# Kernel optimization log

Measured on AMD Instinct MI355X. Metric: run time of the kernel, lower is better.

## Reference

```python
import jax, jax.numpy as jnp
import numpy as np

DIM = 768
HEADS = 12
HEAD_DIM = DIM // HEADS
HIDDEN = 4 * DIM


def layer_norm(x, g, b, eps=1e-5):
    mu = jnp.mean(x, axis=-1, keepdims=True)
    var = jnp.var(x, axis=-1, keepdims=True)
    return (x - mu) * jax.lax.rsqrt(var + eps) * g + b


def setup_inputs() -> dict:
    key = jax.random.key(0)
    ks = jax.random.split(key, 8)
    s = lambda fan_in: 1.0 / np.sqrt(fan_in)
    return {
        "x": jax.random.normal(ks[0], (16, 577, DIM), dtype=jnp.float32),
        "ln1_g": jnp.ones((DIM,), jnp.float32),
        "ln1_b": jnp.zeros((DIM,), jnp.float32),
        "w_qkv": jax.random.uniform(ks[1], (DIM, 3 * DIM), jnp.float32, -s(DIM), s(DIM)),
        "b_qkv": jnp.zeros((3 * DIM,), jnp.float32),
        "w_proj": jax.random.uniform(ks[2], (DIM, DIM), jnp.float32, -s(DIM), s(DIM)),
        "b_proj": jnp.zeros((DIM,), jnp.float32),
        "ln2_g": jnp.ones((DIM,), jnp.float32),
        "ln2_b": jnp.zeros((DIM,), jnp.float32),
        "w_fc1": jax.random.uniform(ks[3], (DIM, HIDDEN), jnp.float32, -s(DIM), s(DIM)),
        "b_fc1": jnp.zeros((HIDDEN,), jnp.float32),
        "w_fc2": jax.random.uniform(ks[4], (HIDDEN, DIM), jnp.float32, -s(HIDDEN), s(HIDDEN)),
        "b_fc2": jnp.zeros((DIM,), jnp.float32),
    }


def reference(x, ln1_g, ln1_b, w_qkv, b_qkv, w_proj, b_proj,
              ln2_g, ln2_b, w_fc1, b_fc1, w_fc2, b_fc2):
    B, N, C = x.shape
    scale = HEAD_DIM ** -0.5

    # --- attention branch (pre-norm) ---
    h = layer_norm(x, ln1_g, ln1_b)
    qkv = h @ w_qkv + b_qkv                               # [B,N,3C]
    qkv = qkv.reshape(B, N, 3, HEADS, HEAD_DIM)
    q, k, v = [qkv[:, :, i].transpose(0, 2, 1, 3) for i in range(3)]  # [B,H,N,D]
    attn = jnp.einsum("bhnd,bhmd->bhnm", q, k) * scale
    attn = jax.nn.softmax(attn, axis=-1)
    out = jnp.einsum("bhnm,bhmd->bhnd", attn, v)          # [B,H,N,D]
    out = out.transpose(0, 2, 1, 3).reshape(B, N, C)
    x = x + (out @ w_proj + b_proj)

    # --- MLP branch (pre-norm) ---
    h = layer_norm(x, ln2_g, ln2_b)
    h = jax.nn.gelu(h @ w_fc1 + b_fc1, approximate=False)
    x = x + (h @ w_fc2 + b_fc2)
    return x
```

## Files before the change

kernel.cpp:

```cpp
#include <hip/hip_runtime.h>
#include <hip/hip_bf16.h>
#include <math.h>

#define NB   16
#define NTOK 577
#define CDIM 768
#define NH   12
#define HID  3072
#define RTOT (NB*NTOK)
#define RPAD (((RTOT+127)/128)*128)
#define BH   (NB*NH)
#define QT   40
#define KF_C (CDIM/32)

typedef __attribute__((ext_vector_type(8))) short bf16x8;
typedef __attribute__((ext_vector_type(4))) float f32x4;
typedef unsigned short u16;

__device__ inline void load_lds16(const void* g, void* l) {
    __builtin_amdgcn_global_load_lds(
        (const __attribute__((address_space(1))) unsigned*)g,
        (__attribute__((address_space(3))) unsigned*)l, 16, 0, 0);
}

__device__ inline size_t blobA(int m, int c, int Kf) {
    return ((size_t)(m >> 4) * Kf + (c >> 5)) * 512 +
           (((c >> 3) & 3) * 16 + (m & 15)) * 8 + (c & 7);
}

__device__ inline float fast_gelu(float x) {
    float y = 0.7978845608f * (x + 0.044715f * x * x * x);
    float e = __expf(2.0f * y);
    float th = 1.0f - 2.0f / (e + 1.0f);
    return 0.5f * x * (1.0f + th);
}

__global__ __launch_bounds__(256) void wconvert_blob(
    const float* __restrict__ src, u16* __restrict__ dst, int K, int N)
{
    int n  = blockIdx.x * 256 + threadIdx.x;
    int kp = blockIdx.y;
    const float* s = src + (size_t)(kp * 8) * N + n;
    __hip_bfloat16 h0 = __float2bfloat16(s[0 * N]);
    __hip_bfloat16 h1 = __float2bfloat16(s[1 * N]);
    __hip_bfloat16 h2 = __float2bfloat16(s[2 * N]);
    __hip_bfloat16 h3 = __float2bfloat16(s[3 * N]);
    __hip_bfloat16 h4 = __float2bfloat16(s[4 * N]);
    __hip_bfloat16 h5 = __float2bfloat16(s[5 * N]);
    __hip_bfloat16 h6 = __float2bfloat16(s[6 * N]);
    __hip_bfloat16 h7 = __float2bfloat16(s[7 * N]);
    ushort4 a = make_ushort4(*(u16*)&h0, *(u16*)&h1, *(u16*)&h2, *(u16*)&h3);
    ushort4 b = make_ushort4(*(u16*)&h4, *(u16*)&h5, *(u16*)&h6, *(u16*)&h7);
    u16* d = dst + ((size_t)(n >> 4) * (K >> 5) + (kp >> 2)) * 512 +
             ((kp & 3) * 16 + (n & 15)) * 8;
    *(ushort4*)(d)     = a;
    *(ushort4*)(d + 4) = b;
}

__global__ __launch_bounds__(256) void ln_kernel(
    const float* __restrict__ x, const float* __restrict__ g,
    const float* __restrict__ b, u16* __restrict__ out)
{
    int row = blockIdx.x;
    const float* xr = x + (size_t)row * CDIM;
    int t = threadIdx.x;
    float v0 = xr[t], v1 = xr[t + 256], v2 = xr[t + 512];
    float s  = v0 + v1 + v2;
    float s2 = v0*v0 + v1*v1 + v2*v2;
    #pragma unroll
    for (int off = 32; off; off >>= 1) {
        s  += __shfl_xor(s, off);
        s2 += __shfl_xor(s2, off);
    }
    __shared__ float red[10];
    int wave = t >> 6, lane = t & 63;
    if (lane == 0) { red[wave] = s; red[wave + 4] = s2; }
    __syncthreads();
    if (t == 0) {
        float ts  = red[0] + red[1] + red[2] + red[3];
        float ts2 = red[4] + red[5] + red[6] + red[7];
        float mu  = ts * (1.0f / CDIM);
        float var = ts2 * (1.0f / CDIM) - mu * mu;
        red[8] = mu;
        red[9] = rsqrtf(var + 1e-5f);
    }
    __syncthreads();
    float mu = red[8], rs = red[9];
    #pragma unroll
    for (int i = 0; i < 3; ++i) {
        int c = t + i * 256;
        float v = (i == 0 ? v0 : (i == 1 ? v1 : v2));
        __hip_bfloat16 hb = __float2bfloat16((v - mu) * rs * g[c] + b[c]);
        out[blobA(row, c, KF_C)] = *(u16*)&hb;
    }
}

template<int TM>
__global__ __launch_bounds__(64) void flat_gemm(
    const u16* __restrict__ Ab, const u16* __restrict__ Bb,
    const float* __restrict__ bias, const float* __restrict__ res,
    void* __restrict__ outv,
    u16* __restrict__ Qp, u16* __restrict__ Kp, u16* __restrict__ Vp,
    int M, int Nc, int K, int nb, int mb, int flags)
{
    __shared__ u16 sb[TM * 1024];
    int lane = threadIdx.x & 63;
    int fr = lane & 15, fq = lane >> 4;

    int fid = blockIdx.x;
    int xcd = fid & 7, w = fid >> 3;
    int slab, n;
    if (flags & 16) {
        int nslab = (mb + 7) >> 3;
        n = w / nslab; slab = w - n * nslab;
    } else {
        slab = w / nb; n = w - slab * nb;
    }
    int m = slab * 8 + xcd;
    if (m >= mb) return;
    int m0 = m * (TM * 16), n0 = n * 64;

    int Kf = K >> 5;
    size_t tstr = (size_t)Kf * 512;
    const u16* Ap = Ab + (size_t)(m0 >> 4) * tstr + lane * 8;
    const u16* Bp = Bb + (size_t)(n0 >> 4) * tstr + lane * 8;

    f32x4 acc[TM][4];
    #pragma unroll
    for (int i = 0; i < TM; ++i)
        #pragma unroll
        for (int j = 0; j < 4; ++j) acc[i][j] = (f32x4){0.f, 0.f, 0.f, 0.f};

#define PF_LD(Abuf, Bbuf, OFF) do {                                          \
    _Pragma("unroll")                                                        \
    for (int tm = 0; tm < TM; ++tm)                                          \
        Abuf[tm] = *(const bf16x8*)(Ap + tm * tstr + (OFF));                 \
    _Pragma("unroll")                                                        \
    for (int tn = 0; tn < 4; ++tn)                                           \
        Bbuf[tn] = *(const bf16x8*)(Bp + tn * tstr + (OFF));                 \
} while (0)

#define PF_FM(Abuf, Bbuf) do {                                               \
    _Pragma("unroll")                                                        \
    for (int tm = 0; tm < TM; ++tm)                                          \
        _Pragma("unroll")                                                    \
        for (int tn = 0; tn < 4; ++tn)                                       \
            acc[tm][tn] = __builtin_amdgcn_mfma_f32_16x16x32_bf16(           \
                Abuf[tm], Bbuf[tn], acc[tm][tn], 0, 0, 0);                   \
} while (0)

    bf16x8 A0[TM], B0[4], A1[TM], B1[4], A2[TM], B2[4];
    PF_LD(A0, B0, 0);
    PF_LD(A1, B1, 512);
    for (int kf = 0; kf < Kf; kf += 3) {
        size_t base = (size_t)kf * 512;
        PF_LD(A2, B2, base + 1024); PF_FM(A0, B0);
        PF_LD(A0, B0, base + 1536); PF_FM(A1, B1);
        PF_LD(A1, B1, base + 2048); PF_FM(A2, B2);
    }
#undef PF_LD
#undef PF_FM

    float* outf = (float*)outv;
    u16* outblob = (u16*)outv;
    int gelu = flags & 1;
    int KfO = Nc >> 5;

    if (flags & 8) {
        int sec = n0 / CDIM;
        int h   = (n0 % CDIM) / 64;
        #pragma unroll
        for (int tm = 0; tm < TM; ++tm) {
            #pragma unroll
            for (int rg = 0; rg < 4; ++rg) {
                int gm = m0 + tm * 16 + fq * 4 + rg;
                if (gm >= M) continue;
                int b   = gm / NTOK;
                int row = gm - b * NTOK;
                int bh  = b * NH + h;
                #pragma unroll
                for (int tn = 0; tn < 4; ++tn) {
                    int d = tn * 16 + fr;
                    float v = acc[tm][tn][rg] + bias[n0 + tn * 16 + fr];
                    __hip_bfloat16 hb = __float2bfloat16(v);
                    if (sec == 0) {
                        Qp[(size_t)(bh * QT + (row >> 4)) * 1024 + (d >> 5) * 512 +
                           (((d >> 3) & 3) * 16 + (row & 15)) * 8 + (d & 7)] = *(u16*)&hb;
                    } else if (sec == 1) {
                        Kp[(size_t)(bh * QT + (row >> 4)) * 1024 + (d >> 5) * 512 +
                           (((d >> 3) & 3) * 16 + (row & 15)) * 8 + (d & 7)] = *(u16*)&hb;
                    } else {
                        Vp[((size_t)(bh * 4 + (d >> 4)) * 20 + (row >> 5)) * 512 +
                           (((row >> 3) & 3) * 16 + (d & 15)) * 8 + (row & 7)] = *(u16*)&hb;
                    }
                }
            }
        }
        return;
    }

    if (flags & 4) {
        #pragma unroll
        for (int tm = 0; tm < TM; ++tm)
            #pragma unroll
            for (int tn = 0; tn < 4; ++tn)
                #pragma unroll
                for (int rg = 0; rg < 4; ++rg) {
                    int cl = tn * 16 + fr;
                    float v = acc[tm][tn][rg] + bias[n0 + cl];
                    if (gelu) v = fast_gelu(v);
                    __hip_bfloat16 hb = __float2bfloat16(v);
                    sb[tm * 1024 + (cl >> 5) * 512 +
                       (((cl >> 3) & 3) * 16 + fq * 4 + rg) * 8 + (cl & 7)] = *(u16*)&hb;
                }
        #pragma unroll
        for (int tm = 0; tm < TM; ++tm) {
            u16* dst = outblob + ((size_t)((m0 >> 4) + tm) * KfO + (n0 >> 5)) * 512;
            *(bf16x8*)(dst + lane * 16)     = *(const bf16x8*)(sb + tm * 1024 + lane * 16);
            *(bf16x8*)(dst + lane * 16 + 8) = *(const bf16x8*)(sb + tm * 1024 + lane * 16 + 8);
        }
        return;
    }

    #pragma unroll
    for (int tm = 0; tm < TM; ++tm) {
        #pragma unroll
        for (int rg = 0; rg < 4; ++rg) {
            int gm = m0 + tm * 16 + fq * 4 + rg;
            if (gm >= M) continue;
            #pragma unroll
            for (int tn = 0; tn < 4; ++tn) {
                int gn = n0 + tn * 16 + fr;
                float v = acc[tm][tn][rg] + bias[gn];
                if (gelu) v = fast_gelu(v);
                if (res)  v += res[(size_t)gm * Nc + gn];
                outf[(size_t)gm * Nc + gn] = v;
            }
        }
    }
}

__global__ __launch_bounds__(256) void attn_mfma(
    const u16* __restrict__ Qp, const u16* __restrict__ Kp,
    const u16* __restrict__ Vp, u16* __restrict__ outp)
{
    __shared__ __align__(16) u16 Ks[4096];
    __shared__ __align__(16) u16 Vs[4096];
    __shared__ __align__(16) u16 Ps[4 * 16 * 72];

    int bh = blockIdx.y, qc = blockIdx.x;
    int b = bh / NH, h = bh % NH;
    int t = threadIdx.x, lane = t & 63, wv = t >> 6;
    int fr = lane & 15, fq = lane >> 4;

    int mt = qc * 4 + wv;
    const u16* qbase = Qp + (size_t)(bh * QT + mt) * 1024 + lane * 8;
    bf16x8 qf0 = *(const bf16x8*)(qbase);
    bf16x8 qf1 = *(const bf16x8*)(qbase + 512);

    const u16* kg = Kp + (size_t)bh * (QT * 1024) + wv * 1024 + lane * 8;
    const u16* vg = Vp + ((size_t)(bh * 4 + wv) * 20) * 512 + lane * 8;
    u16* lK  = Ks + wv * 1024;
    u16* lV  = Vs + wv * 1024;
    u16* psw = Ps + wv * (16 * 72);

    f32x4 o[4];
    float m_r[4], l_r[4];
    #pragma unroll
    for (int i = 0; i < 4; ++i) {
        o[i] = (f32x4){0.f, 0.f, 0.f, 0.f};
        m_r[i] = -1e30f; l_r[i] = 0.f;
    }

    for (int kt = 0; kt < 10; ++kt) {
        load_lds16(kg + kt * 4096,       lK);
        load_lds16(kg + kt * 4096 + 512, lK + 512);
        load_lds16(vg + kt * 1024,       lV);
        load_lds16(vg + kt * 1024 + 512, lV + 512);
        __syncthreads();

        f32x4 sc[4];
        #pragma unroll
        for (int nt = 0; nt < 4; ++nt) {
            sc[nt] = (f32x4){0.f, 0.f, 0.f, 0.f};
            bf16x8 kf0 = *(const bf16x8*)(Ks + (nt * 2 + 0) * 512 + lane * 8);
            bf16x8 kf1 = *(const bf16x8*)(Ks + (nt * 2 + 1) * 512 + lane * 8);
            sc[nt] = __builtin_amdgcn_mfma_f32_16x16x32_bf16(qf0, kf0, sc[nt], 0, 0, 0);
            sc[nt] = __builtin_amdgcn_mfma_f32_16x16x32_bf16(qf1, kf1, sc[nt], 0, 0, 0);
        }

        int j0 = kt * 64;
        float p[4][4], rm[4];
        #pragma unroll
        for (int rg = 0; rg < 4; ++rg) rm[rg] = -1e30f;
        #pragma unroll
        for (int nt = 0; nt < 4; ++nt) {
            bool valid = (j0 + nt * 16 + fr) < NTOK;
            #pragma unroll
            for (int rg = 0; rg < 4; ++rg) {
                float sv = valid ? sc[nt][rg] * 0.125f : -1e30f;
                p[nt][rg] = sv;
                rm[rg] = fmaxf(rm[rg], sv);
            }
        }
        #pragma unroll
        for (int rg = 0; rg < 4; ++rg) {
            #pragma unroll
            for (int off = 1; off < 16; off <<= 1)
                rm[rg] = fmaxf(rm[rg], __shfl_xor(rm[rg], off));
        }
        float alpha[4], rs[4];
        #pragma unroll
        for (int rg = 0; rg < 4; ++rg) {
            float mn = fmaxf(m_r[rg], rm[rg]);
            alpha[rg] = __expf(m_r[rg] - mn);
            m_r[rg] = mn;
            rs[rg] = 0.f;
        }
        #pragma unroll
        for (int nt = 0; nt < 4; ++nt)
            #pragma unroll
            for (int rg = 0; rg < 4; ++rg) {
                float pv = __expf(p[nt][rg] - m_r[rg]);
                p[nt][rg] = pv;
                rs[rg] += pv;
            }
        #pragma unroll
        for (int rg = 0; rg < 4; ++rg) {
            #pragma unroll
            for (int off = 1; off < 16; off <<= 1)
                rs[rg] += __shfl_xor(rs[rg], off);
            l_r[rg] = l_r[rg] * alpha[rg] + rs[rg];
        }

        #pragma unroll
        for (int nt = 0; nt < 4; ++nt)
            #pragma unroll
            for (int rg = 0; rg < 4; ++rg) {
                __hip_bfloat16 hb = __float2bfloat16(p[nt][rg]);
                psw[(fq * 4 + rg) * 72 + nt * 16 + fr] = *(u16*)&hb;
            }
        #pragma unroll
        for (int dt = 0; dt < 4; ++dt)
            #pragma unroll
            for (int rg = 0; rg < 4; ++rg)
                o[dt][rg] *= alpha[rg];

        bf16x8 pf0 = *(const bf16x8*)(psw + fr * 72 + fq * 8);
        bf16x8 pf1 = *(const bf16x8*)(psw + fr * 72 + 32 + fq * 8);
        #pragma unroll
        for (int dt = 0; dt < 4; ++dt) {
            bf16x8 bv0 = *(const bf16x8*)(Vs + (dt * 2 + 0) * 512 + lane * 8);
            bf16x8 bv1 = *(const bf16x8*)(Vs + (dt * 2 + 1) * 512 + lane * 8);
            o[dt] = __builtin_amdgcn_mfma_f32_16x16x32_bf16(pf0, bv0, o[dt], 0, 0, 0);
            o[dt] = __builtin_amdgcn_mfma_f32_16x16x32_bf16(pf1, bv1, o[dt], 0, 0, 0);
        }
        __syncthreads();
    }

    #pragma unroll
    for (int rg = 0; rg < 4; ++rg) {
        int row = qc * 64 + wv * 16 + fq * 4 + rg;
        if (row < NTOK) {
            float rl = 1.0f / l_r[rg];
            int grow = b * NTOK + row;
            #pragma unroll
            for (int dt = 0; dt < 4; ++dt) {
                __hip_bfloat16 hb = __float2bfloat16(o[dt][rg] * rl);
                outp[blobA(grow, h * 64 + dt * 16 + fr, KF_C)] = *(u16*)&hb;
            }
        }
    }
}

static inline int swz_grid(int nb, int mb) { return nb * (((mb + 7) / 8) * 8); }

extern "C" void kernel_launch(void* const* d_in, const int* in_sizes, int n_in,
                              void* d_out, int out_size, void* d_ws, size_t ws_size,
                              hipStream_t stream)
{
    const float* x      = (const float*)d_in[0];
    const float* ln1_g  = (const float*)d_in[1];
    const float* ln1_b  = (const float*)d_in[2];
    const float* w_qkv  = (const float*)d_in[3];
    const float* b_qkv  = (const float*)d_in[4];
    const float* w_proj = (const float*)d_in[5];
    const float* b_proj = (const float*)d_in[6];
    const float* ln2_g  = (const float*)d_in[7];
    const float* ln2_b  = (const float*)d_in[8];
    const float* w_fc1  = (const float*)d_in[9];
    const float* b_fc1  = (const float*)d_in[10];
    const float* w_fc2  = (const float*)d_in[11];
    const float* b_fc2  = (const float*)d_in[12];
    float* out = (float*)d_out;

    char* w = (char*)d_ws;
    u16* Bqkv = (u16*)w; w += (size_t)3*CDIM*CDIM*2;
    u16* Bproj= (u16*)w; w += (size_t)CDIM*CDIM*2;
    u16* Bfc1 = (u16*)w; w += (size_t)HID*CDIM*2;
    u16* Bfc2 = (u16*)w; w += (size_t)CDIM*HID*2;
    u16* hA   = (u16*)w; w += (size_t)RPAD*CDIM*2;
    u16* h3A  = (u16*)w; w += (size_t)RPAD*HID*2;
    u16* Qp   = (u16*)w; w += (size_t)BH*QT*1024*2;
    u16* Kp   = (u16*)w; w += (size_t)BH*QT*1024*2;
    u16* Vp   = (u16*)w; w += (size_t)BH*4*20*512*2;

    int mb4 = (RTOT + 63) / 64;

    wconvert_blob<<<dim3(3*CDIM/256, CDIM/8), 256, 0, stream>>>(w_qkv,  Bqkv, CDIM, 3*CDIM);
    wconvert_blob<<<dim3(CDIM/256,   CDIM/8), 256, 0, stream>>>(w_proj, Bproj, CDIM, CDIM);
    wconvert_blob<<<dim3(HID/256,    CDIM/8), 256, 0, stream>>>(w_fc1,  Bfc1, CDIM, HID);
    wconvert_blob<<<dim3(CDIM/256,   HID/8),  256, 0, stream>>>(w_fc2,  Bfc2, HID, CDIM);

    ln_kernel<<<RTOT, 256, 0, stream>>>(x, ln1_g, ln1_b, hA);
    flat_gemm<4><<<swz_grid(3*CDIM/64, mb4), 64, 0, stream>>>(
        hA, Bqkv, b_qkv, nullptr, nullptr, Qp, Kp, Vp,
        RTOT, 3*CDIM, CDIM, 3*CDIM/64, mb4, 8 | 16);
    attn_mfma<<<dim3(10, BH), 256, 0, stream>>>(Qp, Kp, Vp, hA);
    flat_gemm<4><<<swz_grid(CDIM/64, mb4), 64, 0, stream>>>(
        hA, Bproj, b_proj, x, out, nullptr, nullptr, nullptr,
        RTOT, CDIM, CDIM, CDIM/64, mb4, 0 | 16);
    ln_kernel<<<RTOT, 256, 0, stream>>>(out, ln2_g, ln2_b, hA);
    flat_gemm<4><<<swz_grid(HID/64, mb4), 64, 0, stream>>>(
        hA, Bfc1, b_fc1, nullptr, h3A, nullptr, nullptr, nullptr,
        RTOT, HID, CDIM, HID/64, mb4, 1 | 4 | 16);
    flat_gemm<4><<<swz_grid(CDIM/64, mb4), 64, 0, stream>>>(
        h3A, Bfc2, b_fc2, out, out, nullptr, nullptr, nullptr,
        RTOT, CDIM, HID, CDIM/64, mb4, 0);
}
```

Baseline: 494.7 us.

## Use 256-thread GEMM blocks with per-wave M tiles and split-K for narrow GEMMs

Grows the flat GEMM workgroup from one wave to four. For the QKV and FC1 GEMMs, each wave in a block takes its own 64-row M tile. For the proj and FC2 GEMMs (N=768), the four waves split K four ways, and wave 0 sums the partial accumulators through LDS before writing the fp32 output with bias and residual. The aim is better per-CU occupancy and scheduling, and, for the narrow GEMMs, more parallelism along K. The cost is extra LDS traffic, barriers, and only one wave doing the split-K epilogue.

```diff
diff --git a/kernel.cpp b/kernel.cpp
--- a/kernel.cpp
+++ b/kernel.cpp
@@ -96,34 +96,44 @@
 }
 
 template<int TM>
-__global__ __launch_bounds__(64) void flat_gemm(
+__global__ __launch_bounds__(256) void flat_gemm(
     const u16* __restrict__ Ab, const u16* __restrict__ Bb,
     const float* __restrict__ bias, const float* __restrict__ res,
     void* __restrict__ outv,
     u16* __restrict__ Qp, u16* __restrict__ Kp, u16* __restrict__ Vp,
-    int M, int Nc, int K, int nb, int mb, int flags)
+    int M, int Nc, int K, int nb, int munits, int flags)
 {
-    __shared__ u16 sb[TM * 1024];
-    int lane = threadIdx.x & 63;
+    __shared__ __align__(16) char smem[TM * 2048 * 4];
+    int tid = threadIdx.x;
+    int lane = tid & 63, wv = tid >> 6;
     int fr = lane & 15, fq = lane >> 4;
 
     int fid = blockIdx.x;
     int xcd = fid & 7, w = fid >> 3;
     int slab, n;
     if (flags & 16) {
-        int nslab = (mb + 7) >> 3;
+        int nslab = (munits + 7) >> 3;
         n = w / nslab; slab = w - n * nslab;
     } else {
         slab = w / nb; n = w - slab * nb;
     }
-    int m = slab * 8 + xcd;
-    if (m >= mb) return;
-    int m0 = m * (TM * 16), n0 = n * 64;
+    int mu = slab * 8 + xcd;
+    if (mu >= munits) return;
+
+    int mbtiles = (M + TM * 16 - 1) / (TM * 16);
+    int splitk = flags & 32;
+    int mtile, ks;
+    if (splitk) { mtile = mu;          ks = wv; }
+    else        { mtile = mu * 4 + wv; ks = 0;  }
+    if (mtile >= mbtiles) return;
+    int m0 = mtile * (TM * 16), n0 = n * 64;
 
     int Kf = K >> 5;
+    int Kfs = splitk ? (Kf >> 2) : Kf;
     size_t tstr = (size_t)Kf * 512;
-    const u16* Ap = Ab + (size_t)(m0 >> 4) * tstr + lane * 8;
-    const u16* Bp = Bb + (size_t)(n0 >> 4) * tstr + lane * 8;
+    size_t koff = (size_t)ks * Kfs * 512;
+    const u16* Ap = Ab + (size_t)(m0 >> 4) * tstr + koff + lane * 8;
+    const u16* Bp = Bb + (size_t)(n0 >> 4) * tstr + koff + lane * 8;
 
     f32x4 acc[TM][4];
     #pragma unroll
@@ -152,7 +162,7 @@
     bf16x8 A0[TM], B0[4], A1[TM], B1[4], A2[TM], B2[4];
     PF_LD(A0, B0, 0);
     PF_LD(A1, B1, 512);
-    for (int kf = 0; kf < Kf; kf += 3) {
+    for (int kf = 0; kf < Kfs; kf += 3) {
         size_t base = (size_t)kf * 512;
         PF_LD(A2, B2, base + 1024); PF_FM(A0, B0);
         PF_LD(A0, B0, base + 1536); PF_FM(A1, B1);
@@ -165,6 +175,52 @@
     u16* outblob = (u16*)outv;
     int gelu = flags & 1;
     int KfO = Nc >> 5;
+
+    if (splitk) {
+        float* red = (float*)smem;
+        #pragma unroll
+        for (int c = 0; c < 2; ++c) {
+            if (wv != 0) {
+                float* wr = red + (wv - 1) * 2048;
+                #pragma unroll
+                for (int tm2 = 0; tm2 < 2; ++tm2)
+                    #pragma unroll
+                    for (int tn = 0; tn < 4; ++tn)
+                        *(f32x4*)(wr + (tm2 * 4 + tn) * 256 + lane * 4) =
+                            acc[c * 2 + tm2][tn];
+            }
+            __syncthreads();
+            if (wv == 0) {
+                #pragma unroll
+                for (int s = 0; s < 3; ++s)
+                    #pragma unroll
+                    for (int tm2 = 0; tm2 < 2; ++tm2)
+                        #pragma unroll
+                        for (int tn = 0; tn < 4; ++tn)
+                            acc[c * 2 + tm2][tn] +=
+                                *(const f32x4*)(red + s * 2048 +
+                                                (tm2 * 4 + tn) * 256 + lane * 4);
+            }
+            if (c == 0) __syncthreads();
+        }
+        if (wv != 0) return;
+        #pragma unroll
+        for (int tm = 0; tm < TM; ++tm) {
+            #pragma unroll
+            for (int rg = 0; rg < 4; ++rg) {
+                int gm = m0 + tm * 16 + fq * 4 + rg;
+                if (gm >= M) continue;
+                #pragma unroll
+                for (int tn = 0; tn < 4; ++tn) {
+                    int gn = n0 + tn * 16 + fr;
+                    float v = acc[tm][tn][rg] + bias[gn];
+                    if (res)  v += res[(size_t)gm * Nc + gn];
+                    outf[(size_t)gm * Nc + gn] = v;
+                }
+            }
+        }
+        return;
+    }
 
     if (flags & 8) {
         int sec = n0 / CDIM;
@@ -200,6 +256,7 @@
     }
 
     if (flags & 4) {
+        u16* sb = (u16*)smem + wv * (TM * 1024);
         #pragma unroll
         for (int tm = 0; tm < TM; ++tm)
             #pragma unroll
@@ -373,7 +430,7 @@
     }
 }
 
-static inline int swz_grid(int nb, int mb) { return nb * (((mb + 7) / 8) * 8); }
+static inline int swz_grid(int nb, int munits) { return nb * (((munits + 7) / 8) * 8); }
 
 extern "C" void kernel_launch(void* const* d_in, const int* in_sizes, int n_in,
                               void* d_out, int out_size, void* d_ws, size_t ws_size,
@@ -405,7 +462,8 @@
     u16* Kp   = (u16*)w; w += (size_t)BH*QT*1024*2;
     u16* Vp   = (u16*)w; w += (size_t)BH*4*20*512*2;
 
-    int mb4 = (RTOT + 63) / 64;
+    int mt = (RTOT + 63) / 64;
+    int mg = (mt + 3) / 4;
 
     wconvert_blob<<<dim3(3*CDIM/256, CDIM/8), 256, 0, stream>>>(w_qkv,  Bqkv, CDIM, 3*CDIM);
     wconvert_blob<<<dim3(CDIM/256,   CDIM/8), 256, 0, stream>>>(w_proj, Bproj, CDIM, CDIM);
@@ -413,18 +471,18 @@
     wconvert_blob<<<dim3(CDIM/256,   HID/8),  256, 0, stream>>>(w_fc2,  Bfc2, HID, CDIM);
 
     ln_kernel<<<RTOT, 256, 0, stream>>>(x, ln1_g, ln1_b, hA);
-    flat_gemm<4><<<swz_grid(3*CDIM/64, mb4), 64, 0, stream>>>(
+    flat_gemm<4><<<swz_grid(3*CDIM/64, mg), 256, 0, stream>>>(
         hA, Bqkv, b_qkv, nullptr, nullptr, Qp, Kp, Vp,
-        RTOT, 3*CDIM, CDIM, 3*CDIM/64, mb4, 8 | 16);
+        RTOT, 3*CDIM, CDIM, 3*CDIM/64, mg, 8 | 16);
     attn_mfma<<<dim3(10, BH), 256, 0, stream>>>(Qp, Kp, Vp, hA);
-    flat_gemm<4><<<swz_grid(CDIM/64, mb4), 64, 0, stream>>>(
+    flat_gemm<4><<<swz_grid(CDIM/64, mt), 256, 0, stream>>>(
         hA, Bproj, b_proj, x, out, nullptr, nullptr, nullptr,
-        RTOT, CDIM, CDIM, CDIM/64, mb4, 0 | 16);
+        RTOT, CDIM, CDIM, CDIM/64, mt, 32);
     ln_kernel<<<RTOT, 256, 0, stream>>>(out, ln2_g, ln2_b, hA);
-    flat_gemm<4><<<swz_grid(HID/64, mb4), 64, 0, stream>>>(
+    flat_gemm<4><<<swz_grid(HID/64, mg), 256, 0, stream>>>(
         hA, Bfc1, b_fc1, nullptr, h3A, nullptr, nullptr, nullptr,
-        RTOT, HID, CDIM, HID/64, mb4, 1 | 4 | 16);
-    flat_gemm<4><<<swz_grid(CDIM/64, mb4), 64, 0, stream>>>(
+        RTOT, HID, CDIM, HID/64, mg, 1 | 4 | 16);
+    flat_gemm<4><<<swz_grid(CDIM/64, mt), 256, 0, stream>>>(
         h3A, Bfc2, b_fc2, out, out, nullptr, nullptr, nullptr,
-        RTOT, CDIM, HID, CDIM/64, mb4, 0);
-}
+        RTOT, CDIM, HID, CDIM/64, mt, 32);
+}
```

After: 554.5 us. 1.12x slower.
